# Performance work log

Measured on AMD Instinct MI355X. Metric: run time of the kernel, lower is better.

## Reference

```python
import jax, jax.numpy as jnp
import numpy as np

N = 100000
E = 1600000
NEG_SLOPE_ATTN = 0.2   # DGL GATConv default negative_slope
NEG_SLOPE_ACT = 0.01   # F.leaky_relu default


def gat_conv(x, src, dst, W, al, ar, b):
    """DGL-style GATConv with a single head.
    x: [N, Fin]; W: [Fin, H*Fout]; al, ar: [H, Fout]; b: [H*Fout].
    Returns [N, H, Fout]."""
    H, Fout = al.shape
    h = (x @ W).reshape(-1, H, Fout)                 # [N,H,Fout]
    el = jnp.sum(h * al, axis=-1)                    # [N,H]
    er = jnp.sum(h * ar, axis=-1)                    # [N,H]
    e = jax.nn.leaky_relu(el[src] + er[dst], NEG_SLOPE_ATTN)  # [E,H]
    # edge softmax over incoming edges of each dst node
    m = jax.ops.segment_max(e, dst, num_segments=N)  # [N,H]
    ex = jnp.exp(e - m[dst])                         # [E,H]
    denom = jax.ops.segment_sum(ex, dst, num_segments=N)      # [N,H]
    a = ex / denom[dst]                              # [E,H]
    msg = h[src] * a[:, :, None]                     # [E,H,Fout]
    out = jax.ops.segment_sum(msg, dst, num_segments=N)       # [N,H,Fout]
    return out + b.reshape(1, H, Fout)


def setup_inputs() -> dict:
    key = jax.random.key(0)
    ks = jax.random.split(key, 16)
    features = jax.random.normal(ks[0], (N, 3), dtype=jnp.float32)
    src = jax.random.randint(ks[1], (E,), 0, N)
    dst = jax.random.randint(ks[2], (E,), 0, N)

    def glorot(k, shape):
        fan = shape[0] + shape[-1]
        s = jnp.sqrt(2.0 / fan).astype(jnp.float32)
        return jax.random.normal(k, shape, dtype=jnp.float32) * s

    W1 = glorot(ks[3], (3, 64));   al1 = glorot(ks[4], (1, 64));  ar1 = glorot(ks[5], (1, 64));  b1 = jnp.zeros((64,), jnp.float32)
    W2 = glorot(ks[6], (64, 64));  al2 = glorot(ks[7], (1, 64));  ar2 = glorot(ks[8], (1, 64));  b2 = jnp.zeros((64,), jnp.float32)
    W3 = glorot(ks[9], (64, 3));   al3 = glorot(ks[10], (1, 3));  ar3 = glorot(ks[11], (1, 3));  b3 = jnp.zeros((3,), jnp.float32)
    return {"features": features, "src": src, "dst": dst,
            "W1": W1, "al1": al1, "ar1": ar1, "b1": b1,
            "W2": W2, "al2": al2, "ar2": ar2, "b2": b2,
            "W3": W3, "al3": al3, "ar3": ar3, "b3": b3}


def reference(features, src, dst, W1, al1, ar1, b1, W2, al2, ar2, b2, W3, al3, ar3, b3):
    x = gat_conv(features, src, dst, W1, al1, ar1, b1)      # [N,1,64]
    x = jax.nn.leaky_relu(x, NEG_SLOPE_ACT)
    x = gat_conv(x[:, 0, :], src, dst, W2, al2, ar2, b2)     # [N,1,64]
    x = jax.nn.leaky_relu(x, NEG_SLOPE_ACT)
    x = gat_conv(x[:, 0, :], src, dst, W3, al3, ar3, b3)     # [N,1,3]
    return x[:, 0, :]                                        # [N,3]
```

## Files before the change

### kernel.cpp

```cpp
#include <hip/hip_runtime.h>
#include <hip/hip_fp16.h>
#include <math.h>


#define NEG_BIG (-1e30f)
#define SORT_CAP 6144
#define BSTRIDE 6144
#define CHUNK 8192

__device__ inline float waveSum(float v) {
#pragma unroll
  for (int off = 32; off; off >>= 1) v += __shfl_xor(v, off, 64);
  return v;
}

__device__ inline float halfSum(float v) {
#pragma unroll
  for (int off = 16; off; off >>= 1) v += __shfl_xor(v, off, 64);
  return v;
}

__device__ inline float halfMax(float v) {
#pragma unroll
  for (int off = 16; off; off >>= 1) v = fmaxf(v, __shfl_xor(v, off, 64));
  return v;
}

__device__ inline int waveMaxI(int v) {
#pragma unroll
  for (int off = 32; off; off >>= 1) v = max(v, __shfl_xor(v, off, 64));
  return v;
}

__device__ inline int rlI(int v, int l) { return __builtin_amdgcn_readlane(v, l); }
__device__ inline float rlF(float v, int l) {
  return __int_as_float(__builtin_amdgcn_readlane(__float_as_int(v), l));
}
__device__ inline int ntI(const int* p) { return __builtin_nontemporal_load(p); }

__global__ __launch_bounds__(1024) void k_bin(
    const int* __restrict__ src, const int* __restrict__ dst,
    int* __restrict__ gcursor, unsigned* __restrict__ binned, int E, int NBK) {
  __shared__ int lcnt[512];
  __shared__ int lbase[512];
  int tid = threadIdx.x;
  for (int b = tid; b < NBK; b += 1024) lcnt[b] = 0;
  __syncthreads();
  int e0 = blockIdx.x * CHUNK;
  int e1 = min(e0 + CHUNK, E);
  for (int e = e0 + tid; e < e1; e += 1024)
    atomicAdd(&lcnt[ntI(&dst[e]) >> 8], 1);
  __syncthreads();
  for (int b = tid; b < NBK; b += 1024) {
    int c = lcnt[b];
    lbase[b] = c ? atomicAdd(&gcursor[b], c) : 0;
    lcnt[b] = 0;
  }
  __syncthreads();
  for (int e = e0 + tid; e < e1; e += 1024) {
    int dd = ntI(&dst[e]);
    int ss = ntI(&src[e]);
    int b = dd >> 8;
    int pos = lbase[b] + atomicAdd(&lcnt[b], 1);
    if (pos < BSTRIDE)
      binned[(size_t)b * BSTRIDE + pos] =
          ((unsigned)(dd & 255) << 24) | (unsigned)ss;
  }
}

__global__ void k_bscan(const int* __restrict__ cnt, int* __restrict__ base,
                        int NBK, int E, int* __restrict__ startv, int N) {
  __shared__ int s[1024];
  int t = threadIdx.x;
  int v = (t < NBK) ? cnt[t] : 0;
  s[t] = v;
  __syncthreads();
  for (int off = 1; off < 1024; off <<= 1) {
    int u = (t >= off) ? s[t - off] : 0;
    __syncthreads();
    s[t] += u;
    __syncthreads();
  }
  int excl = s[t] - v;
  if (t <= NBK) base[t] = excl;
  if (t == 0) startv[N] = E;
}

__global__ __launch_bounds__(256) void k_sort(
    const unsigned* __restrict__ binned, const int* __restrict__ base,
    int* __restrict__ csr, int* __restrict__ startv, int N) {
  __shared__ unsigned sbuf[SORT_CAP];
  __shared__ unsigned obuf[SORT_CAP];
  __shared__ int hist[256];
  __shared__ int scn[256];
  __shared__ int cur[256];
  int b = blockIdx.x;
  int tid = threadIdx.x;
  int gbase = base[b];
  int cnt = min(base[b + 1] - gbase, BSTRIDE);
  const unsigned* bsrc = binned + (size_t)b * BSTRIDE;
  hist[tid] = 0;
  __syncthreads();
  if (cnt <= SORT_CAP) {
    for (int i = tid; i < cnt; i += 256) {
      unsigned w = bsrc[i];
      sbuf[i] = w;
      atomicAdd(&hist[w >> 24], 1);
    }
    __syncthreads();
    int v = hist[tid];
    scn[tid] = v;
    __syncthreads();
    for (int off = 1; off < 256; off <<= 1) {
      int u = (tid >= off) ? scn[tid - off] : 0;
      __syncthreads();
      scn[tid] += u;
      __syncthreads();
    }
    int excl = scn[tid] - v;
    cur[tid] = excl;
    int dn = b * 256 + tid;
    if (dn < N) startv[dn] = gbase + excl;
    __syncthreads();
    for (int i = tid; i < cnt; i += 256) {
      unsigned w = sbuf[i];
      int p = atomicAdd(&cur[w >> 24], 1);
      obuf[p] = w & 0xFFFFFFu;
    }
    __syncthreads();
    for (int i = tid; i < cnt; i += 256) csr[gbase + i] = (int)obuf[i];
  } else {
    for (int i = tid; i < cnt; i += 256)
      atomicAdd(&hist[bsrc[i] >> 24], 1);
    __syncthreads();
    int v = hist[tid];
    scn[tid] = v;
    __syncthreads();
    for (int off = 1; off < 256; off <<= 1) {
      int u = (tid >= off) ? scn[tid - off] : 0;
      __syncthreads();
      scn[tid] += u;
      __syncthreads();
    }
    int excl = scn[tid] - v;
    cur[tid] = excl;
    int dn = b * 256 + tid;
    if (dn < N) startv[dn] = gbase + excl;
    __syncthreads();
    for (int i = tid; i < cnt; i += 256) {
      unsigned w = bsrc[i];
      int p = atomicAdd(&cur[w >> 24], 1);
      csr[gbase + p] = (int)(w & 0xFFFFFFu);
    }
  }
}

__global__ void k_prep(const float* __restrict__ W1, const float* __restrict__ al1,
                       const float* __restrict__ ar1, const float* __restrict__ W2,
                       const float* __restrict__ al2, const float* __restrict__ ar2,
                       float* __restrict__ uvw) {
  int lane = threadIdx.x & 63;
  float a = al1[lane], r = ar1[lane];
#pragma unroll
  for (int i = 0; i < 3; ++i) {
    float w = W1[i * 64 + lane];
    float ui = waveSum(w * a);
    float vi = waveSum(w * r);
    if (lane == 0) { uvw[i] = ui; uvw[3 + i] = vi; }
  }
  float sa = 0.f, sr = 0.f;
  for (int j = 0; j < 64; ++j) {
    float w = W2[lane * 64 + j];
    sa = fmaf(w, al2[j], sa);
    sr = fmaf(w, ar2[j], sr);
  }
  uvw[8 + lane] = sa;
  uvw[72 + lane] = sr;
}

__global__ void k_padx(const float* __restrict__ x, const float* __restrict__ uvw,
                       float4* __restrict__ x4, float* __restrict__ er1, int N) {
  int n = blockIdx.x * blockDim.x + threadIdx.x;
  if (n >= N) return;
  float x0 = __builtin_nontemporal_load(&x[n * 3]);
  float x1 = __builtin_nontemporal_load(&x[n * 3 + 1]);
  float x2 = __builtin_nontemporal_load(&x[n * 3 + 2]);
  float el = fmaf(x0, uvw[0], fmaf(x1, uvw[1], x2 * uvw[2]));
  float er = fmaf(x0, uvw[3], fmaf(x1, uvw[4], x2 * uvw[5]));
  x4[n] = make_float4(x0, x1, x2, el);
  er1[n] = er;
}

__global__ __launch_bounds__(256) void k_agg1x(
    const float4* __restrict__ x4, const float* __restrict__ er1,
    const float* __restrict__ W1, const float* __restrict__ b1,
    const int* __restrict__ start, const int* __restrict__ csr,
    __half* __restrict__ x2, int N) {
  int tid = threadIdx.x;
  int wave = tid >> 6, lane = tid & 63, hl = lane & 31, half = lane >> 5;
  int pA = blockIdx.x * 8 + wave * 2;
  int pn = pA + half;
  int n = (pn < N) ? pn : 0;
  int beg = start[n], end = start[n + 1];
  float ern = er1[n];
  float m = NEG_BIG, d = 0.f, X0 = 0.f, X1 = 0.f, X2 = 0.f;
  for (int base = beg; base < end; base += 32) {
    int idx = base + hl;
    int s = (idx < end) ? ntI(&csr[idx]) : 0;
    s = ((unsigned)s < (unsigned)N) ? s : 0;
    float4 hv = x4[s];
    float e = hv.w + ern;
    e = e > 0.f ? e : 0.2f * e;
    e = (idx < end) ? e : NEG_BIG;
    float mn = fmaxf(m, halfMax(e));
    float sc = __expf(m - mn);
    float q = __expf(e - mn);
    d = d * sc + halfSum(q);
    X0 = X0 * sc + halfSum(q * hv.x);
    X1 = X1 * sc + halfSum(q * hv.y);
    X2 = X2 * sc + halfSum(q * hv.z);
    m = mn;
  }
  float inv = (end > beg) ? 1.f / d : 0.f;
  X0 *= inv; X1 *= inv; X2 *= inv;
  float A0 = rlF(X0, 0), A1 = rlF(X1, 0), A2 = rlF(X2, 0);
  float B0 = rlF(X0, 32), B1 = rlF(X1, 32), B2 = rlF(X2, 32);
  float w1a = W1[lane], w1b = W1[64 + lane], w1c = W1[128 + lane];
  float bb = b1[lane];
  if (pA < N) {
    float vA = fmaf(A0, w1a, fmaf(A1, w1b, fmaf(A2, w1c, bb)));
    vA = vA > 0.f ? vA : 0.01f * vA;
    x2[(size_t)pA * 64 + lane] = __float2half(vA);
  }
  int pB = pA + 1;
  if (pB < N) {
    float vB = fmaf(B0, w1a, fmaf(B1, w1b, fmaf(B2, w1c, bb)));
    vB = vB > 0.f ? vB : 0.01f * vB;
    x2[(size_t)pB * 64 + lane] = __float2half(vB);
  }
}

__global__ __launch_bounds__(256) void k_gemm2(const __half* x2_in,
                                               const float* __restrict__ W2,
                                               const float* __restrict__ uvw,
                                               __half* h2_out,
                                               float* __restrict__ el2,
                                               float* __restrict__ er2, int N) {
  __shared__ float sW[64 * 64];
  __shared__ float sX[64 * 64];
  __shared__ float swal[64];
  __shared__ float swar[64];
  int tid = threadIdx.x;
  for (int i = tid; i < 4096; i += 256) sW[i] = W2[i];
  if (tid < 64) swal[tid] = uvw[8 + tid];
  else if (tid < 128) swar[tid - 64] = uvw[72 + tid - 64];
  const unsigned* xu = (const unsigned*)x2_in;
  size_t base = (size_t)blockIdx.x * 2048;
  size_t limit = (size_t)N * 32;
  for (int i = tid; i < 2048; i += 256) {
    size_t gi = base + i;
    unsigned u = (gi < limit) ? __builtin_nontemporal_load(&xu[gi]) : 0u;
    __half2 hh = *(__half2*)&u;
    float2 f = __half22float2(hh);
    sX[2 * i] = f.x;
    sX[2 * i + 1] = f.y;
  }
  __syncthreads();
  int wave = tid >> 6, f = tid & 63;
  int r0 = wave * 16;
  float acc[16];
#pragma unroll
  for (int i = 0; i < 16; ++i) acc[i] = 0.f;
  const float2* sX2 = (const float2*)sX;
  for (int k2 = 0; k2 < 32; ++k2) {
    float wv0 = sW[(2 * k2) * 64 + f];
    float wv1 = sW[(2 * k2 + 1) * 64 + f];
#pragma unroll
    for (int i = 0; i < 16; ++i) {
      float2 xv = sX2[(r0 + i) * 32 + k2];
      acc[i] = fmaf(xv.x, wv0, fmaf(xv.y, wv1, acc[i]));
    }
  }
  if (tid < 64) {
    float sa = 0.f, sr = 0.f;
#pragma unroll 8
    for (int k = 0; k < 64; ++k) {
      float xv = sX[tid * 64 + k];
      sa = fmaf(xv, swal[k], sa);
      sr = fmaf(xv, swar[k], sr);
    }
    int row = blockIdx.x * 64 + tid;
    if (row < N) { el2[row] = sa; er2[row] = sr; }
  }
  int rowbase = blockIdx.x * 64 + r0;
#pragma unroll
  for (int i = 0; i < 16; ++i) {
    int row = rowbase + i;
    if (row < N) h2_out[(size_t)row * 64 + f] = __float2half(acc[i]);
  }
}

__global__ __launch_bounds__(256) void k_agg2f(
    const __half* __restrict__ h2, const float* __restrict__ el,
    const float* __restrict__ er, const int* __restrict__ start,
    const int* __restrict__ csr, const float* __restrict__ b2,
    const float* __restrict__ W3, const float* __restrict__ al3,
    float* __restrict__ h3, int N) {
  __shared__ int2 sSA[4][64];
  int tid = threadIdx.x;
  int wave = tid >> 6, lane = tid & 63, hl = lane & 31, half = lane >> 5;
  int pn = blockIdx.x * 8 + wave * 2 + half;
  int n = (pn < N) ? pn : 0;
  int beg = start[n], end = start[n + 1];
  int deg = end - beg;
  int maxd = __builtin_amdgcn_readfirstlane(waveMaxI(deg));
  float ern = er[n];
  float ox = 0.f, oy = 0.f;

  int sA = 0; float aA = 0.f;
  if (maxd <= 32) {
    int idx = beg + hl;
    int s = (idx < end) ? ntI(&csr[idx]) : 0;
    s = ((unsigned)s < (unsigned)N) ? s : 0;
    float e = el[s] + ern;
    e = e > 0.f ? e : 0.2f * e;
    e = (idx < end) ? e : NEG_BIG;
    float mm = halfMax(e);
    float q = __expf(e - mm);
    float dsum = halfSum(q);
    float inv = (deg > 0) ? 1.f / dsum : 0.f;
    sA = s; aA = q * inv;
  }
  sSA[wave][half * 32 + hl] = make_int2(sA, __float_as_int(aA));
  __syncthreads();

  if (maxd <= 32) {
    const int2* sp = &sSA[wave][half * 32];
    for (int j = 0; j < maxd; j += 4) {
#pragma unroll
      for (int k = 0; k < 4; ++k) {
        int2 w = sp[j + k];
        int sj = w.x;
        float aj = __int_as_float(w.y);
        const __half2* hp = (const __half2*)(h2 + (size_t)sj * 64);
        float2 hf = __half22float2(hp[hl]);
        ox = fmaf(aj, hf.x, ox);
        oy = fmaf(aj, hf.y, oy);
      }
    }
  } else {
    float m = NEG_BIG, dsum = 0.f;
    for (int base = beg; base < end; base += 32) {
      int idx = base + hl;
      int s = (idx < end) ? csr[idx] : 0;
      s = ((unsigned)s < (unsigned)N) ? s : 0;
      float e = el[s] + ern;
      e = e > 0.f ? e : 0.2f * e;
      e = (idx < end) ? e : NEG_BIG;
      float mn = fmaxf(m, halfMax(e));
      dsum = dsum * __expf(m - mn) + halfSum(__expf(e - mn));
      m = mn;
    }
    float inv = (deg > 0) ? 1.f / dsum : 0.f;
    for (int base = beg; base < end; base += 32) {
      int idx = base + hl;
      int s = (idx < end) ? csr[idx] : 0;
      s = ((unsigned)s < (unsigned)N) ? s : 0;
      float e = el[s] + ern;
      e = e > 0.f ? e : 0.2f * e;
      float a = (idx < end) ? __expf(e - m) * inv : 0.f;
      for (int j = 0; j < 32; ++j) {
        int sAx = rlI(s, j), sBx = rlI(s, j + 32);
        float aAx = rlF(a, j), aBx = rlF(a, j + 32);
        int sj = half ? sBx : sAx;
        float aj = half ? aBx : aAx;
        const __half2* hp = (const __half2*)(h2 + (size_t)sj * 64);
        float2 hf = __half22float2(hp[hl]);
        ox = fmaf(aj, hf.x, ox);
        oy = fmaf(aj, hf.y, oy);
      }
    }
  }
  float2 bb = ((const float2*)b2)[hl];
  float r0 = ox + bb.x, r1 = oy + bb.y;
  r0 = r0 > 0.f ? r0 : 0.01f * r0;
  r1 = r1 > 0.f ? r1 : 0.01f * r1;
  int k0 = 2 * hl, k1 = 2 * hl + 1;
  float p0 = halfSum(fmaf(r0, W3[k0 * 3 + 0], r1 * W3[k1 * 3 + 0]));
  float p1 = halfSum(fmaf(r0, W3[k0 * 3 + 1], r1 * W3[k1 * 3 + 1]));
  float p2 = halfSum(fmaf(r0, W3[k0 * 3 + 2], r1 * W3[k1 * 3 + 2]));
  if (hl == 0 && pn < N) {
    float el3 = fmaf(p0, al3[0], fmaf(p1, al3[1], p2 * al3[2]));
    h3[n * 4 + 0] = p0; h3[n * 4 + 1] = p1; h3[n * 4 + 2] = p2; h3[n * 4 + 3] = el3;
  }
}

__global__ __launch_bounds__(256) void k_agg3(
    const float4* __restrict__ h3, const int* __restrict__ start,
    const int* __restrict__ csr, const float* __restrict__ ar3,
    const float* __restrict__ b, float* __restrict__ out, int N) {
  int tid = threadIdx.x;
  int wave = tid >> 6, lane = tid & 63, hl = lane & 31, half = lane >> 5;
  int pn = blockIdx.x * 8 + wave * 2 + half;
  int n = (pn < N) ? pn : 0;
  int beg = start[n], end = start[n + 1];
  float4 hn = h3[n];
  float ern = fmaf(hn.x, ar3[0], fmaf(hn.y, ar3[1], hn.z * ar3[2]));
  float m = NEG_BIG, d = 0.f, Q0 = 0.f, Q1 = 0.f, Q2 = 0.f;
  for (int base = beg; base < end; base += 32) {
    int idx = base + hl;
    int s = (idx < end) ? ntI(&csr[idx]) : 0;
    s = ((unsigned)s < (unsigned)N) ? s : 0;
    float4 hv = h3[s];
    float e = hv.w + ern;
    e = e > 0.f ? e : 0.2f * e;
    e = (idx < end) ? e : NEG_BIG;
    float mn = fmaxf(m, halfMax(e));
    float sc = __expf(m - mn);
    float q = __expf(e - mn);
    d = d * sc + halfSum(q);
    Q0 = Q0 * sc + halfSum(q * hv.x);
    Q1 = Q1 * sc + halfSum(q * hv.y);
    Q2 = Q2 * sc + halfSum(q * hv.z);
    m = mn;
  }
  float inv = (end > beg) ? 1.f / d : 0.f;
  if (hl == 0 && pn < N) {
    out[n * 3 + 0] = fmaf(Q0, inv, b[0]);
    out[n * 3 + 1] = fmaf(Q1, inv, b[1]);
    out[n * 3 + 2] = fmaf(Q2, inv, b[2]);
  }
}

extern "C" void kernel_launch(void* const* d_in, const int* in_sizes, int n_in,
                              void* d_out, int out_size, void* d_ws, size_t ws_size,
                              hipStream_t stream) {
  const int N = in_sizes[0] / 3;
  const int E = in_sizes[1];
  const float* feats = (const float*)d_in[0];
  const int* src = (const int*)d_in[1];
  const int* dst = (const int*)d_in[2];
  const float* W1  = (const float*)d_in[3];
  const float* al1 = (const float*)d_in[4];
  const float* ar1 = (const float*)d_in[5];
  const float* b1  = (const float*)d_in[6];
  const float* W2  = (const float*)d_in[7];
  const float* al2 = (const float*)d_in[8];
  const float* ar2 = (const float*)d_in[9];
  const float* b2  = (const float*)d_in[10];
  const float* W3  = (const float*)d_in[11];
  const float* al3 = (const float*)d_in[12];
  const float* ar3 = (const float*)d_in[13];
  const float* b3  = (const float*)d_in[14];

  const int NBK = (N + 255) >> 8;

  char* ws = (char*)d_ws;
  size_t off = 0;
  auto alloc = [&](size_t bytes) -> void* {
    void* p = ws + off;
    off = (off + bytes + 255) & ~(size_t)255;
    return p;
  };
  int* startv  = (int*)alloc((size_t)(N + 1) * 4);
  int* csr     = (int*)alloc((size_t)E * 4);
  float* elB   = (float*)alloc((size_t)N * 4);
  float* erB   = (float*)alloc((size_t)N * 4);
  float* er1   = (float*)alloc((size_t)N * 4);
  int* gcount  = (int*)alloc((size_t)NBK * 4);
  int* baseb   = (int*)alloc((size_t)(NBK + 1) * 4);
  float* uvw   = (float*)alloc(1024);
  float* h3    = (float*)alloc((size_t)N * 4 * 4);
  float4* x4   = (float4*)alloc((size_t)N * 16);
  __half* x2   = (__half*)alloc((size_t)N * 64 * 2);
  unsigned* binned = (unsigned*)x2;

  const int NB  = (N + 255) / 256;
  const int NB8 = (N + 7) / 8;
  const int GB  = (N + 63) / 64;
  const int CB  = (E + CHUNK - 1) / CHUNK;

  k_prep<<<1, 64, 0, stream>>>(W1, al1, ar1, W2, al2, ar2, uvw);
  k_padx<<<NB, 256, 0, stream>>>(feats, uvw, x4, er1, N);

  hipMemsetAsync(gcount, 0, (size_t)NBK * 4, stream);
  k_bin<<<CB, 1024, 0, stream>>>(src, dst, gcount, binned, E, NBK);
  k_bscan<<<1, 1024, 0, stream>>>(gcount, baseb, NBK, E, startv, N);
  k_sort<<<NBK, 256, 0, stream>>>(binned, baseb, csr, startv, N);

  k_agg1x<<<NB8, 256, 0, stream>>>(x4, er1, W1, b1, startv, csr, x2, N);
  k_gemm2<<<GB, 256, 0, stream>>>(x2, W2, uvw, x2, elB, erB, N);
  k_agg2f<<<NB8, 256, 0, stream>>>(x2, elB, erB, startv, csr, b2, W3, al3, h3, N);
  k_agg3<<<NB8, 256, 0, stream>>>((const float4*)h3, startv, csr, ar3, b3,
                                  (float*)d_out, N);
}
```

Before: 246.2 us.

## Aggregate layer-2 on compact 3-wide inputs, apply W2 after aggregation

Layer-1 aggregation now writes only the 3-float aggregated vector plus the layer-2 attention logits (el2/er2, computed through wave reductions) instead of the 64-wide half-precision activations. Layer-2 aggregation gathers these 16-byte records per edge and recomputes the 64-wide layer-1 activation on the fly, then aggregates. W2 is applied after aggregation, using linearity, in a GEMM kernel that also fuses the bias, leaky-ReLU and the W3/al3 projection. This replaces 128-byte gathers per edge with 16-byte gathers, at the cost of extra per-edge ALU work and an extra intermediate array.

```diff
diff --git a/kernel.cpp b/kernel.cpp
--- a/kernel.cpp
+++ b/kernel.cpp
@@ -194,8 +194,9 @@
 __global__ __launch_bounds__(256) void k_agg1x(
     const float4* __restrict__ x4, const float* __restrict__ er1,
     const float* __restrict__ W1, const float* __restrict__ b1,
-    const int* __restrict__ start, const int* __restrict__ csr,
-    __half* __restrict__ x2, int N) {
+    const float* __restrict__ uvw, const int* __restrict__ start,
+    const int* __restrict__ csr, float4* __restrict__ a4,
+    float* __restrict__ er2, int N) {
   int tid = threadIdx.x;
   int wave = tid >> 6, lane = tid & 63, hl = lane & 31, half = lane >> 5;
   int pA = blockIdx.x * 8 + wave * 2;
@@ -227,34 +228,128 @@
   float B0 = rlF(X0, 32), B1 = rlF(X1, 32), B2 = rlF(X2, 32);
   float w1a = W1[lane], w1b = W1[64 + lane], w1c = W1[128 + lane];
   float bb = b1[lane];
-  if (pA < N) {
-    float vA = fmaf(A0, w1a, fmaf(A1, w1b, fmaf(A2, w1c, bb)));
-    vA = vA > 0.f ? vA : 0.01f * vA;
-    x2[(size_t)pA * 64 + lane] = __float2half(vA);
-  }
-  int pB = pA + 1;
-  if (pB < N) {
-    float vB = fmaf(B0, w1a, fmaf(B1, w1b, fmaf(B2, w1c, bb)));
-    vB = vB > 0.f ? vB : 0.01f * vB;
-    x2[(size_t)pB * 64 + lane] = __float2half(vB);
-  }
-}
-
-__global__ __launch_bounds__(256) void k_gemm2(const __half* x2_in,
-                                               const float* __restrict__ W2,
-                                               const float* __restrict__ uvw,
-                                               __half* h2_out,
-                                               float* __restrict__ el2,
-                                               float* __restrict__ er2, int N) {
+  float vA = fmaf(A0, w1a, fmaf(A1, w1b, fmaf(A2, w1c, bb)));
+  vA = vA > 0.f ? vA : 0.01f * vA;
+  float vB = fmaf(B0, w1a, fmaf(B1, w1b, fmaf(B2, w1c, bb)));
+  vB = vB > 0.f ? vB : 0.01f * vB;
+  float wal = uvw[8 + lane], war = uvw[72 + lane];
+  float eA = waveSum(vA * wal);
+  float rA = waveSum(vA * war);
+  float eB = waveSum(vB * wal);
+  float rB = waveSum(vB * war);
+  if (lane == 0) {
+    if (pA < N) { a4[pA] = make_float4(A0, A1, A2, eA); er2[pA] = rA; }
+    int pB = pA + 1;
+    if (pB < N) { a4[pB] = make_float4(B0, B1, B2, eB); er2[pB] = rB; }
+  }
+}
+
+__global__ __launch_bounds__(256) void k_agg2r(
+    const float4* __restrict__ a4, const float* __restrict__ er2,
+    const int* __restrict__ start, const int* __restrict__ csr,
+    const float* __restrict__ W1, const float* __restrict__ b1,
+    __half* __restrict__ xa, int N) {
+  __shared__ float4 sAV[4][64];
+  int tid = threadIdx.x;
+  int wave = tid >> 6, lane = tid & 63, hl = lane & 31, half = lane >> 5;
+  int pn = blockIdx.x * 8 + wave * 2 + half;
+  int n = (pn < N) ? pn : 0;
+  int beg = start[n], end = start[n + 1];
+  int deg = end - beg;
+  int maxd = __builtin_amdgcn_readfirstlane(waveMaxI(deg));
+  float ern = er2[n];
+  int k0 = 2 * hl;
+  float wa0 = W1[k0],     wb0 = W1[64 + k0],     wc0 = W1[128 + k0],     bb0 = b1[k0];
+  float wa1 = W1[k0 + 1], wb1 = W1[64 + k0 + 1], wc1 = W1[128 + k0 + 1], bb1 = b1[k0 + 1];
+  float acc0 = 0.f, acc1 = 0.f;
+
+  float aA = 0.f, v0s = 0.f, v1s = 0.f, v2s = 0.f;
+  if (maxd <= 32) {
+    int idx = beg + hl;
+    int s = (idx < end) ? ntI(&csr[idx]) : 0;
+    s = ((unsigned)s < (unsigned)N) ? s : 0;
+    float4 av = a4[s];
+    float e = av.w + ern;
+    e = e > 0.f ? e : 0.2f * e;
+    e = (idx < end) ? e : NEG_BIG;
+    float mm = halfMax(e);
+    float q = __expf(e - mm);
+    float dsum = halfSum(q);
+    float inv = (deg > 0) ? 1.f / dsum : 0.f;
+    aA = q * inv;
+    v0s = av.x; v1s = av.y; v2s = av.z;
+  }
+  sAV[wave][half * 32 + hl] = make_float4(aA, v0s, v1s, v2s);
+  __syncthreads();
+
+  if (maxd <= 32) {
+    const float4* sp = &sAV[wave][half * 32];
+    for (int j = 0; j < maxd; j += 4) {
+#pragma unroll
+      for (int k = 0; k < 4; ++k) {
+        float4 w = sp[j + k];
+        float a = w.x;
+        float v0 = fmaf(w.w, wc0, fmaf(w.z, wb0, fmaf(w.y, wa0, bb0)));
+        v0 = v0 > 0.f ? v0 : 0.01f * v0;
+        float v1 = fmaf(w.w, wc1, fmaf(w.z, wb1, fmaf(w.y, wa1, bb1)));
+        v1 = v1 > 0.f ? v1 : 0.01f * v1;
+        acc0 = fmaf(a, v0, acc0);
+        acc1 = fmaf(a, v1, acc1);
+      }
+    }
+  } else {
+    float m = NEG_BIG, dsum = 0.f;
+    for (int base = beg; base < end; base += 32) {
+      int idx = base + hl;
+      int s = (idx < end) ? csr[idx] : 0;
+      s = ((unsigned)s < (unsigned)N) ? s : 0;
+      float e = a4[s].w + ern;
+      e = e > 0.f ? e : 0.2f * e;
+      e = (idx < end) ? e : NEG_BIG;
+      float mn = fmaxf(m, halfMax(e));
+      dsum = dsum * __expf(m - mn) + halfSum(__expf(e - mn));
+      m = mn;
+    }
+    float inv = (deg > 0) ? 1.f / dsum : 0.f;
+    for (int base = beg; base < end; base += 32) {
+      int idx = base + hl;
+      int s = (idx < end) ? csr[idx] : 0;
+      s = ((unsigned)s < (unsigned)N) ? s : 0;
+      float e = a4[s].w + ern;
+      e = e > 0.f ? e : 0.2f * e;
+      float a = (idx < end) ? __expf(e - m) * inv : 0.f;
+      for (int j = 0; j < 32; ++j) {
+        int sAx = rlI(s, j), sBx = rlI(s, j + 32);
+        float aAx = rlF(a, j), aBx = rlF(a, j + 32);
+        int sj = half ? sBx : sAx;
+        float aj = half ? aBx : aAx;
+        float4 av = a4[sj];
+        float v0 = fmaf(av.z, wc0, fmaf(av.y, wb0, fmaf(av.x, wa0, bb0)));
+        v0 = v0 > 0.f ? v0 : 0.01f * v0;
+        float v1 = fmaf(av.z, wc1, fmaf(av.y, wb1, fmaf(av.x, wa1, bb1)));
+        v1 = v1 > 0.f ? v1 : 0.01f * v1;
+        acc0 = fmaf(aj, v0, acc0);
+        acc1 = fmaf(aj, v1, acc1);
+      }
+    }
+  }
+  if (pn < N) {
+    __half2 hv = __float22half2_rn(make_float2(acc0, acc1));
+    ((__half2*)xa)[(size_t)pn * 32 + hl] = hv;
+  }
+}
+
+__global__ __launch_bounds__(256) void k_gemm3(
+    const __half* xa_in, const float* __restrict__ W2,
+    const float* __restrict__ b2, const float* __restrict__ W3,
+    const float* __restrict__ al3, float* __restrict__ h3, int N) {
   __shared__ float sW[64 * 64];
   __shared__ float sX[64 * 64];
-  __shared__ float swal[64];
-  __shared__ float swar[64];
+  __shared__ float sW3[192];
   int tid = threadIdx.x;
   for (int i = tid; i < 4096; i += 256) sW[i] = W2[i];
-  if (tid < 64) swal[tid] = uvw[8 + tid];
-  else if (tid < 128) swar[tid - 64] = uvw[72 + tid - 64];
-  const unsigned* xu = (const unsigned*)x2_in;
+  if (tid < 192) sW3[tid] = W3[tid];
+  const unsigned* xu = (const unsigned*)xa_in;
   size_t base = (size_t)blockIdx.x * 2048;
   size_t limit = (size_t)N * 32;
   for (int i = tid; i < 2048; i += 256) {
@@ -281,118 +376,29 @@
       acc[i] = fmaf(xv.x, wv0, fmaf(xv.y, wv1, acc[i]));
     }
   }
-  if (tid < 64) {
-    float sa = 0.f, sr = 0.f;
-#pragma unroll 8
-    for (int k = 0; k < 64; ++k) {
-      float xv = sX[tid * 64 + k];
-      sa = fmaf(xv, swal[k], sa);
-      sr = fmaf(xv, swar[k], sr);
-    }
-    int row = blockIdx.x * 64 + tid;
-    if (row < N) { el2[row] = sa; er2[row] = sr; }
-  }
-  int rowbase = blockIdx.x * 64 + r0;
+  float bf = b2[f];
+  __syncthreads();
 #pragma unroll
   for (int i = 0; i < 16; ++i) {
-    int row = rowbase + i;
-    if (row < N) h2_out[(size_t)row * 64 + f] = __float2half(acc[i]);
-  }
-}
-
-__global__ __launch_bounds__(256) void k_agg2f(
-    const __half* __restrict__ h2, const float* __restrict__ el,
-    const float* __restrict__ er, const int* __restrict__ start,
-    const int* __restrict__ csr, const float* __restrict__ b2,
-    const float* __restrict__ W3, const float* __restrict__ al3,
-    float* __restrict__ h3, int N) {
-  __shared__ int2 sSA[4][64];
-  int tid = threadIdx.x;
-  int wave = tid >> 6, lane = tid & 63, hl = lane & 31, half = lane >> 5;
-  int pn = blockIdx.x * 8 + wave * 2 + half;
-  int n = (pn < N) ? pn : 0;
-  int beg = start[n], end = start[n + 1];
-  int deg = end - beg;
-  int maxd = __builtin_amdgcn_readfirstlane(waveMaxI(deg));
-  float ern = er[n];
-  float ox = 0.f, oy = 0.f;
-
-  int sA = 0; float aA = 0.f;
-  if (maxd <= 32) {
-    int idx = beg + hl;
-    int s = (idx < end) ? ntI(&csr[idx]) : 0;
-    s = ((unsigned)s < (unsigned)N) ? s : 0;
-    float e = el[s] + ern;
-    e = e > 0.f ? e : 0.2f * e;
-    e = (idx < end) ? e : NEG_BIG;
-    float mm = halfMax(e);
-    float q = __expf(e - mm);
-    float dsum = halfSum(q);
-    float inv = (deg > 0) ? 1.f / dsum : 0.f;
-    sA = s; aA = q * inv;
-  }
-  sSA[wave][half * 32 + hl] = make_int2(sA, __float_as_int(aA));
-  __syncthreads();
-
-  if (maxd <= 32) {
-    const int2* sp = &sSA[wave][half * 32];
-    for (int j = 0; j < maxd; j += 4) {
-#pragma unroll
-      for (int k = 0; k < 4; ++k) {
-        int2 w = sp[j + k];
-        int sj = w.x;
-        float aj = __int_as_float(w.y);
-        const __half2* hp = (const __half2*)(h2 + (size_t)sj * 64);
-        float2 hf = __half22float2(hp[hl]);
-        ox = fmaf(aj, hf.x, ox);
-        oy = fmaf(aj, hf.y, oy);
-      }
-    }
-  } else {
-    float m = NEG_BIG, dsum = 0.f;
-    for (int base = beg; base < end; base += 32) {
-      int idx = base + hl;
-      int s = (idx < end) ? csr[idx] : 0;
-      s = ((unsigned)s < (unsigned)N) ? s : 0;
-      float e = el[s] + ern;
-      e = e > 0.f ? e : 0.2f * e;
-      e = (idx < end) ? e : NEG_BIG;
-      float mn = fmaxf(m, halfMax(e));
-      dsum = dsum * __expf(m - mn) + halfSum(__expf(e - mn));
-      m = mn;
-    }
-    float inv = (deg > 0) ? 1.f / dsum : 0.f;
-    for (int base = beg; base < end; base += 32) {
-      int idx = base + hl;
-      int s = (idx < end) ? csr[idx] : 0;
-      s = ((unsigned)s < (unsigned)N) ? s : 0;
-      float e = el[s] + ern;
-      e = e > 0.f ? e : 0.2f * e;
-      float a = (idx < end) ? __expf(e - m) * inv : 0.f;
-      for (int j = 0; j < 32; ++j) {
-        int sAx = rlI(s, j), sBx = rlI(s, j + 32);
-        float aAx = rlF(a, j), aBx = rlF(a, j + 32);
-        int sj = half ? sBx : sAx;
-        float aj = half ? aBx : aAx;
-        const __half2* hp = (const __half2*)(h2 + (size_t)sj * 64);
-        float2 hf = __half22float2(hp[hl]);
-        ox = fmaf(aj, hf.x, ox);
-        oy = fmaf(aj, hf.y, oy);
-      }
-    }
-  }
-  float2 bb = ((const float2*)b2)[hl];
-  float r0 = ox + bb.x, r1 = oy + bb.y;
-  r0 = r0 > 0.f ? r0 : 0.01f * r0;
-  r1 = r1 > 0.f ? r1 : 0.01f * r1;
-  int k0 = 2 * hl, k1 = 2 * hl + 1;
-  float p0 = halfSum(fmaf(r0, W3[k0 * 3 + 0], r1 * W3[k1 * 3 + 0]));
-  float p1 = halfSum(fmaf(r0, W3[k0 * 3 + 1], r1 * W3[k1 * 3 + 1]));
-  float p2 = halfSum(fmaf(r0, W3[k0 * 3 + 2], r1 * W3[k1 * 3 + 2]));
-  if (hl == 0 && pn < N) {
-    float el3 = fmaf(p0, al3[0], fmaf(p1, al3[1], p2 * al3[2]));
-    h3[n * 4 + 0] = p0; h3[n * 4 + 1] = p1; h3[n * 4 + 2] = p2; h3[n * 4 + 3] = el3;
-  }
+    float r = acc[i] + bf;
+    r = r > 0.f ? r : 0.01f * r;
+    sX[(r0 + i) * 64 + f] = r;
+  }
+  __syncthreads();
+  int row = tid >> 2, j = tid & 3;
+  int j3 = (j < 3) ? j : 0;
+  float p = 0.f;
+  for (int i = 0; i < 64; ++i) {
+    int ff = (row + i) & 63;
+    p = fmaf(sX[row * 64 + ff], sW3[ff * 3 + j3], p);
+  }
+  int lb = (tid & 63) & ~3;
+  float q0 = __shfl(p, lb + 0, 64);
+  float q1 = __shfl(p, lb + 1, 64);
+  float q2 = __shfl(p, lb + 2, 64);
+  float val = (j < 3) ? p : fmaf(q0, al3[0], fmaf(q1, al3[1], q2 * al3[2]));
+  int grow = blockIdx.x * 64 + row;
+  if (grow < N) h3[(size_t)blockIdx.x * 256 + tid] = val;
 }
 
 __global__ __launch_bounds__(256) void k_agg3(
@@ -464,16 +470,16 @@
   };
   int* startv  = (int*)alloc((size_t)(N + 1) * 4);
   int* csr     = (int*)alloc((size_t)E * 4);
-  float* elB   = (float*)alloc((size_t)N * 4);
-  float* erB   = (float*)alloc((size_t)N * 4);
+  float* er2v  = (float*)alloc((size_t)N * 4);
   float* er1   = (float*)alloc((size_t)N * 4);
   int* gcount  = (int*)alloc((size_t)NBK * 4);
   int* baseb   = (int*)alloc((size_t)(NBK + 1) * 4);
   float* uvw   = (float*)alloc(1024);
   float* h3    = (float*)alloc((size_t)N * 4 * 4);
   float4* x4   = (float4*)alloc((size_t)N * 16);
-  __half* x2   = (__half*)alloc((size_t)N * 64 * 2);
-  unsigned* binned = (unsigned*)x2;
+  float4* a4   = (float4*)alloc((size_t)N * 16);
+  __half* xa   = (__half*)alloc((size_t)N * 64 * 2);
+  unsigned* binned = (unsigned*)xa;
 
   const int NB  = (N + 255) / 256;
   const int NB8 = (N + 7) / 8;
@@ -488,9 +494,10 @@
   k_bscan<<<1, 1024, 0, stream>>>(gcount, baseb, NBK, E, startv, N);
   k_sort<<<NBK, 256, 0, stream>>>(binned, baseb, csr, startv, N);
 
-  k_agg1x<<<NB8, 256, 0, stream>>>(x4, er1, W1, b1, startv, csr, x2, N);
-  k_gemm2<<<GB, 256, 0, stream>>>(x2, W2, uvw, x2, elB, erB, N);
-  k_agg2f<<<NB8, 256, 0, stream>>>(x2, elB, erB, startv, csr, b2, W3, al3, h3, N);
+  k_agg1x<<<NB8, 256, 0, stream>>>(x4, er1, W1, b1, uvw, startv, csr,
+                                   a4, er2v, N);
+  k_agg2r<<<NB8, 256, 0, stream>>>(a4, er2v, startv, csr, W1, b1, xa, N);
+  k_gemm3<<<GB, 256, 0, stream>>>(xa, W2, b2, W3, al3, h3, N);
   k_agg3<<<NB8, 256, 0, stream>>>((const float4*)h3, startv, csr, ar3, b3,
                                   (float*)d_out, N);
 }
```

Measured after the change: 243.6 us. Within noise of the previous version (-1.1%).
